# Optimization experiments

Measured on AMD Instinct MI355X. Metric: run time of the kernel, lower is better.

The kernel has to match this reference:

```python
import jax, jax.numpy as jnp
import numpy as np

N, D, H, E, K = 4096, 512, 2048, 8, 2  # tokens, input_size, hidden_size, num_experts, top_k


def setup_inputs() -> dict:
    key = jax.random.key(0)
    ks = jax.random.split(key, 4)
    x = jax.random.normal(ks[0], (N, D), dtype=jnp.float32)
    # torch init: weights ~ N(0, 0.001), biases zero
    Wg = jax.random.normal(ks[1], (D, E), dtype=jnp.float32) * 0.001
    bg = jnp.zeros((E,), jnp.float32)
    W1 = jax.random.normal(ks[2], (E, D, H), dtype=jnp.float32) * 0.001
    b1 = jnp.zeros((E, H), jnp.float32)
    W2 = jax.random.normal(ks[3], (E, H, D), dtype=jnp.float32) * 0.001
    b2 = jnp.zeros((E, D), jnp.float32)
    return {"x": x, "Wg": Wg, "bg": bg, "W1": W1, "b1": b1, "W2": W2, "b2": b2}


def reference(x, Wg, bg, W1, b1, W2, b2):
    # Gating: softmax over experts
    gates = jax.nn.softmax(x @ Wg + bg, axis=-1)            # [N, E]
    top_w, top_i = jax.lax.top_k(gates, K)                  # [N, K]
    top_w = top_w / jnp.sum(top_w, axis=-1, keepdims=True)  # renormalize

    # Expert MLP (fc1 -> fc2, no nonlinearity per source). Vectorized across all
    # experts, then gather the top-k selected outputs per token.
    h1 = jnp.einsum('nd,edh->neh', x, W1) + b1              # [N, E, H]
    all_out = jnp.einsum('neh,ehd->ned', h1, W2) + b2       # [N, E, D]
    sel = jnp.take_along_axis(all_out, top_i[:, :, None], axis=1)  # [N, K, D]

    combined = jnp.einsum('nkd,nk->nd', sel, top_w)         # [N, D]

    # usage counts: scatter-add of (detached) top-k weights per expert
    usage = jnp.zeros((E,), x.dtype).at[top_i.reshape(-1)].add(
        jax.lax.stop_gradient(top_w).reshape(-1))
    return combined, usage
```

## Files before the change

kernel.cpp:

```cpp
#include <hip/hip_runtime.h>
#include <hip/hip_bf16.h>


#define N_TOK 4096
#define DIM   512
#define HID   2048
#define NEXP  8
#define TOTSLOT (2 * N_TOK)
#define M1TILE 72
#define M2TILE 144
#define NGATE  256

typedef __attribute__((ext_vector_type(8))) short short8;
typedef __attribute__((ext_vector_type(4))) float f32x4;

static __device__ __forceinline__ unsigned short f2bf(float f) {
    __hip_bfloat16 b = __float2bfloat16(f);
    return *reinterpret_cast<unsigned short*>(&b);
}
static __device__ __forceinline__ float bf2f(unsigned short u) {
    return __uint_as_float((unsigned)u << 16);
}

static __device__ __forceinline__ void load16_to_lds(const void* g, void* l) {
    __builtin_amdgcn_global_load_lds(
        (const __attribute__((address_space(1))) unsigned int*)g,
        (__attribute__((address_space(3))) unsigned int*)l, 16, 0, 0);
}

__global__ __launch_bounds__(256) void prep_kernel(
    const float* __restrict__ W1, const float* __restrict__ W2,
    unsigned short* __restrict__ W1t, unsigned short* __restrict__ W2t,
    const float* __restrict__ x, const float* __restrict__ Wg,
    const float* __restrict__ bg,
    int* __restrict__ te, float* __restrict__ tw,
    int* __restrict__ pcnt, float* __restrict__ pus,
    unsigned short* __restrict__ Xb)
{
    int bid = blockIdx.x;
    int tid = threadIdx.x;

    if (bid < 4096) {
        __shared__ unsigned short tile[64][65];
        int z = bid >> 8, bx = bid & 255;
        const float* in; unsigned short* outp; int R, C, rt, ct, e;
        if (z < NEXP) { e = z;        in = W1; outp = W1t; R = DIM; C = HID; rt = bx >> 5; ct = bx & 31; }
        else          { e = z - NEXP; in = W2; outp = W2t; R = HID; C = DIM; rt = bx >> 3; ct = bx & 7;  }
        const float* src = in + (size_t)e * R * C;
        unsigned short* dst = outp + (size_t)e * R * C;
        int r0 = rt * 64, c0 = ct * 64;
        int rr = tid >> 2, cb = (tid & 3) * 16;
#pragma unroll
        for (int i = 0; i < 4; ++i) {
            float4 v = *(const float4*)&src[(size_t)(r0 + rr) * C + c0 + cb + i * 4];
            tile[rr][cb + i * 4 + 0] = f2bf(v.x);
            tile[rr][cb + i * 4 + 1] = f2bf(v.y);
            tile[rr][cb + i * 4 + 2] = f2bf(v.z);
            tile[rr][cb + i * 4 + 3] = f2bf(v.w);
        }
        __syncthreads();
#pragma unroll
        for (int i = 0; i < 4; ++i) {
            ushort4 u;
            u.x = tile[cb + i * 4 + 0][rr];
            u.y = tile[cb + i * 4 + 1][rr];
            u.z = tile[cb + i * 4 + 2][rr];
            u.w = tile[cb + i * 4 + 3][rr];
            *(ushort4*)&dst[(size_t)(c0 + rr) * R + r0 + cb + i * 4] = u;
        }
        return;
    }

    __shared__ int   lcnt[NEXP];
    __shared__ float lus[NEXP];
    int g = bid - 4096;
    if (tid < NEXP) { lcnt[tid] = 0; lus[tid] = 0.f; }
    __syncthreads();

    int wave = tid >> 6;
    int lane = tid & 63;

    for (int t = 0; t < 4; ++t) {
        int n = g * 16 + wave * 4 + t;

        float acc[NEXP];
#pragma unroll
        for (int e = 0; e < NEXP; ++e) acc[e] = 0.f;

#pragma unroll
        for (int it = 0; it < DIM / 64; ++it) {
            int d = it * 64 + lane;
            float xv = x[n * DIM + d];
            Xb[n * DIM + d] = f2bf(xv);
            float4 wa = *(const float4*)&Wg[d * NEXP];
            float4 wb = *(const float4*)&Wg[d * NEXP + 4];
            acc[0] += xv * wa.x; acc[1] += xv * wa.y;
            acc[2] += xv * wa.z; acc[3] += xv * wa.w;
            acc[4] += xv * wb.x; acc[5] += xv * wb.y;
            acc[6] += xv * wb.z; acc[7] += xv * wb.w;
        }
#pragma unroll
        for (int m = 32; m >= 1; m >>= 1) {
#pragma unroll
            for (int e = 0; e < NEXP; ++e)
                acc[e] += __shfl_xor(acc[e], m, 64);
        }
        if (lane == 0) {
            float l[NEXP];
#pragma unroll
            for (int e = 0; e < NEXP; ++e) l[e] = acc[e] + bg[e];
            int i0 = 0;
#pragma unroll
            for (int e = 1; e < NEXP; ++e) if (l[e] > l[i0]) i0 = e;
            int i1 = (i0 == 0) ? 1 : 0;
#pragma unroll
            for (int e = 0; e < NEXP; ++e)
                if (e != i0 && l[e] > l[i1]) i1 = e;
            float w0 = 1.f / (1.f + expf(l[i1] - l[i0]));
            float w1 = 1.f - w0;
            te[n * 2] = i0; te[n * 2 + 1] = i1;
            tw[n * 2] = w0; tw[n * 2 + 1] = w1;
            atomicAdd(&lcnt[i0], 1);
            atomicAdd(&lcnt[i1], 1);
            atomicAdd(&lus[i0], w0);
            atomicAdd(&lus[i1], w1);
        }
    }
    __syncthreads();
    if (tid < NEXP) {
        pcnt[g * NEXP + tid] = lcnt[tid];
        pus[g * NEXP + tid]  = lus[tid];
    }
}

__global__ __launch_bounds__(256) void scatter_kernel(
    int* __restrict__ te, const float* __restrict__ tw,
    const int* __restrict__ pcnt, const float* __restrict__ pus,
    int* __restrict__ btok, float* __restrict__ bwt,
    int* __restrict__ cnt, int* __restrict__ offs,
    int* __restrict__ tb128, int* __restrict__ tb64, int* __restrict__ ntile,
    float* __restrict__ usage)
{
    __shared__ int pc[NGATE * NEXP];
    __shared__ int cnt_s[NEXP], off_s[NEXP], base_s[NEXP], lrank[NEXP];
    int tid = threadIdx.x, b = blockIdx.x;

    {
        const int4* src = (const int4*)pcnt;
        int4* dst = (int4*)pc;
        dst[tid]       = src[tid];
        dst[tid + 256] = src[tid + 256];
    }
    if (tid < NEXP) lrank[tid] = 0;
    __syncthreads();

    if (tid < NEXP) {
        int e = tid, s = 0, pre = 0;
        for (int g = 0; g < NGATE; ++g) {
            int v = pc[g * NEXP + e];
            if (g < b * 16) pre += v;
            s += v;
        }
        cnt_s[e] = s; base_s[e] = pre;
    }
    __syncthreads();
    if (tid == 0) {
        int o = 0;
        for (int e = 0; e < NEXP; ++e) { off_s[e] = o; o += cnt_s[e]; }
    }
    __syncthreads();
    if (tid < NEXP) base_s[tid] += off_s[tid];

    if (b == 0) {
        if (tid < NEXP) {
            cnt[tid] = cnt_s[tid]; offs[tid] = off_s[tid];
            float s = 0.f;
            for (int g = 0; g < NGATE; ++g) s += pus[g * NEXP + tid];
            usage[tid] = s;
        }
        if (tid == 0) {
            int a = 0, bb = 0;
            for (int e = 0; e < NEXP; ++e) {
                tb128[e] = a; a += (cnt_s[e] + 127) >> 7;
                tb64[e]  = bb; bb += (cnt_s[e] + 63) >> 6;
            }
            tb128[NEXP] = a; tb64[NEXP] = bb;
            ntile[0] = a; ntile[1] = bb;
        }
    }
    __syncthreads();

    int n = b * 256 + tid;
    int e0 = te[n * 2], e1 = te[n * 2 + 1];
    int l0 = atomicAdd(&lrank[e0], 1);
    int l1 = atomicAdd(&lrank[e1], 1);
    int s0 = base_s[e0] + l0;
    int s1 = base_s[e1] + l1;
    btok[s0] = n; bwt[s0] = tw[n * 2];
    btok[s1] = n; bwt[s1] = tw[n * 2 + 1];
    te[n * 2] = s0; te[n * 2 + 1] = s1;
}


__global__ __launch_bounds__(256) void gemm1_kernel(
    const unsigned short* __restrict__ Xb, const unsigned short* __restrict__ W1t,
    const float* __restrict__ b1, const int* __restrict__ cnt,
    const int* __restrict__ offs, const int* __restrict__ btok,
    const int* __restrict__ tb128, const int* __restrict__ ntile,
    unsigned short* __restrict__ H1)
{
    __shared__ __align__(16) unsigned short Ws[2][128 * 64];
    __shared__ __align__(16) unsigned short Xs[2][128 * 64];
    __shared__ int tok_s[128];

    int bx = blockIdx.x;
    int ti = (bx & 7) * (M1TILE / 8) + (bx >> 3);
    if (ti >= ntile[0]) return;
    int e = 0;
#pragma unroll
    for (int k = 1; k < NEXP; ++k) if (ti >= tb128[k]) e = k;
    int tt = ti - tb128[e];
    int ht = blockIdx.y;
    int cn = cnt[e];
    int off_e = offs[e];
    int tid = threadIdx.x;

    if (tid < 128) {
        int lr = tt * 128 + tid;
        tok_s[tid] = (lr < cn) ? btok[off_e + lr] : 0;
    }
    __syncthreads();

    int wave = tid >> 6, lane = tid & 63;
    int mbase = (wave >> 1) * 64, nbase = (wave & 1) * 64;
    int quad = lane >> 4, lcol = lane & 15;
    f32x4 acc[4][4];
#pragma unroll
    for (int mi = 0; mi < 4; ++mi)
#pragma unroll
        for (int ni = 0; ni < 4; ++ni)
            acc[mi][ni] = (f32x4){0.f, 0.f, 0.f, 0.f};

    int Rb = tid >> 3, pc = tid & 7;
    const unsigned short* Wsrc = W1t + ((size_t)e * HID + ht * 128) * DIM;

    auto stage = [&](int buf, int k0) {
#pragma unroll
        for (int p = 0; p < 4; ++p) {
            int R = Rb + p * 32;
            int c = pc ^ (R & 7);
            load16_to_lds(&Wsrc[(size_t)R * DIM + k0 + c * 8], &Ws[buf][R * 64 + pc * 8]);
            load16_to_lds(&Xb[(size_t)tok_s[R] * DIM + k0 + c * 8], &Xs[buf][R * 64 + pc * 8]);
        }
    };

    stage(0, 0);

    const int NT = DIM / 64;
    for (int t = 0; t < NT; ++t) {
        int cur = t & 1;
        if (t + 1 < NT) {
            stage(cur ^ 1, (t + 1) * 64);
            asm volatile("s_waitcnt vmcnt(8)" ::: "memory");
        } else {
            asm volatile("s_waitcnt vmcnt(0)" ::: "memory");
        }
        __builtin_amdgcn_s_barrier();
        __builtin_amdgcn_sched_barrier(0);
#pragma unroll
        for (int h = 0; h < 2; ++h) {
            int cs = ((h * 4 + quad) ^ (lcol & 7)) * 8;
            short8 a[4], b[4];
#pragma unroll
            for (int i = 0; i < 4; ++i) {
                a[i] = *(const short8*)&Ws[cur][(mbase + i * 16 + lcol) * 64 + cs];
                b[i] = *(const short8*)&Xs[cur][(nbase + i * 16 + lcol) * 64 + cs];
            }
#pragma unroll
            for (int mi = 0; mi < 4; ++mi)
#pragma unroll
                for (int ni = 0; ni < 4; ++ni)
                    acc[mi][ni] = __builtin_amdgcn_mfma_f32_16x16x32_bf16(
                        a[mi], b[ni], acc[mi][ni], 0, 0, 0);
        }
        __builtin_amdgcn_sched_barrier(0);
        __builtin_amdgcn_s_barrier();
    }

    float4 bv[4];
#pragma unroll
    for (int mi = 0; mi < 4; ++mi)
        bv[mi] = *(const float4*)&b1[e * HID + ht * 128 + mbase + mi * 16 + quad * 4];
#pragma unroll
    for (int ni = 0; ni < 4; ++ni) {
        int tn = tt * 128 + nbase + ni * 16 + lcol;
        if (tn >= cn) continue;
        size_t srow = (size_t)(off_e + tn) * HID + ht * 128;
#pragma unroll
        for (int mi = 0; mi < 4; ++mi) {
            int hh = mbase + mi * 16 + quad * 4;
            ushort4 u;
            u.x = f2bf(acc[mi][ni][0] + bv[mi].x);
            u.y = f2bf(acc[mi][ni][1] + bv[mi].y);
            u.z = f2bf(acc[mi][ni][2] + bv[mi].z);
            u.w = f2bf(acc[mi][ni][3] + bv[mi].w);
            *(ushort4*)&H1[srow + hh] = u;
        }
    }
}

__global__ __launch_bounds__(256) void gemm2_kernel(
    const unsigned short* __restrict__ H1, const unsigned short* __restrict__ W2t,
    const float* __restrict__ b2, const int* __restrict__ cnt,
    const int* __restrict__ offs, const float* __restrict__ bwt,
    const int* __restrict__ tb64, const int* __restrict__ ntile,
    unsigned short* __restrict__ O)
{
    __shared__ __align__(16) unsigned short Ws[2][128 * 64];
    __shared__ __align__(16) unsigned short Hs[2][64 * 64];
    __shared__ float wt_s[64];

    int bx = blockIdx.x;
    int ti = (bx & 7) * (M2TILE / 8) + (bx >> 3);
    if (ti >= ntile[1]) return;
    int e = 0;
#pragma unroll
    for (int k = 1; k < NEXP; ++k) if (ti >= tb64[k]) e = k;
    int tt = ti - tb64[e];
    int dt = blockIdx.y;
    int cn = cnt[e];
    int off_e = offs[e];
    int sb = off_e + tt * 64;
    int tid = threadIdx.x;

    if (tid < 64) {
        int lr = tt * 64 + tid;
        wt_s[tid] = (lr < cn) ? bwt[off_e + lr] : 0.f;
    }

    int wave = tid >> 6, lane = tid & 63;
    int nbase = wave * 32;
    int quad = lane >> 4, lcol = lane & 15;
    f32x4 acc[4][2];
#pragma unroll
    for (int mi = 0; mi < 4; ++mi)
#pragma unroll
        for (int ni = 0; ni < 2; ++ni)
            acc[mi][ni] = (f32x4){0.f, 0.f, 0.f, 0.f};

    int Rb = tid >> 3, pc = tid & 7;
    const unsigned short* Wsrc = W2t + ((size_t)e * DIM + dt * 128) * HID;

    auto stage = [&](int buf, int k0) {
#pragma unroll
        for (int p = 0; p < 4; ++p) {
            int R = Rb + p * 32;
            int c = pc ^ (R & 7);
            load16_to_lds(&Wsrc[(size_t)R * HID + k0 + c * 8], &Ws[buf][R * 64 + pc * 8]);
        }
#pragma unroll
        for (int p = 0; p < 2; ++p) {
            int R = Rb + p * 32;
            int c = pc ^ (R & 7);
            int sr = sb + R; if (sr > TOTSLOT - 1) sr = TOTSLOT - 1;
            load16_to_lds(&H1[(size_t)sr * HID + k0 + c * 8], &Hs[buf][R * 64 + pc * 8]);
        }
    };

    stage(0, 0);

    const int NT = HID / 64;
    for (int t = 0; t < NT; ++t) {
        int cur = t & 1;
        if (t + 1 < NT) {
            stage(cur ^ 1, (t + 1) * 64);
            asm volatile("s_waitcnt vmcnt(6)" ::: "memory");
        } else {
            asm volatile("s_waitcnt vmcnt(0)" ::: "memory");
        }
        __builtin_amdgcn_s_barrier();
        __builtin_amdgcn_sched_barrier(0);
#pragma unroll
        for (int h = 0; h < 2; ++h) {
            int cs = ((h * 4 + quad) ^ (lcol & 7)) * 8;
            short8 a[4], b[2];
#pragma unroll
            for (int i = 0; i < 4; ++i)
                a[i] = *(const short8*)&Hs[cur][(i * 16 + lcol) * 64 + cs];
#pragma unroll
            for (int i = 0; i < 2; ++i)
                b[i] = *(const short8*)&Ws[cur][(nbase + i * 16 + lcol) * 64 + cs];
#pragma unroll
            for (int mi = 0; mi < 4; ++mi)
#pragma unroll
                for (int ni = 0; ni < 2; ++ni)
                    acc[mi][ni] = __builtin_amdgcn_mfma_f32_16x16x32_bf16(
                        a[mi], b[ni], acc[mi][ni], 0, 0, 0);
        }
        __builtin_amdgcn_sched_barrier(0);
        __builtin_amdgcn_s_barrier();
    }

    unsigned short* Oe = O + (size_t)sb * DIM + dt * 128;
#pragma unroll
    for (int ni = 0; ni < 2; ++ni) {
        int dl = nbase + ni * 16 + lcol;
        float bv = b2[e * DIM + dt * 128 + dl];
#pragma unroll
        for (int mi = 0; mi < 4; ++mi) {
            int rl = mi * 16 + quad * 4;
#pragma unroll
            for (int r = 0; r < 4; ++r) {
                int sl = rl + r;
                if (tt * 64 + sl < cn)
                    Oe[(size_t)sl * DIM + dl] = f2bf(wt_s[sl] * (acc[mi][ni][r] + bv));
            }
        }
    }
}

__global__ __launch_bounds__(256) void combine_kernel(
    const unsigned short* __restrict__ O, const int* __restrict__ sidx,
    float* __restrict__ out)
{
    int tid = threadIdx.x;
    int n = blockIdx.x * 2 + (tid >> 7);
    int dd = (tid & 127) * 4;
    int s0 = sidx[n * 2], s1 = sidx[n * 2 + 1];
    ushort4 a = *(const ushort4*)&O[(size_t)s0 * DIM + dd];
    ushort4 c = *(const ushort4*)&O[(size_t)s1 * DIM + dd];
    float4 o;
    o.x = bf2f(a.x) + bf2f(c.x);
    o.y = bf2f(a.y) + bf2f(c.y);
    o.z = bf2f(a.z) + bf2f(c.z);
    o.w = bf2f(a.w) + bf2f(c.w);
    *(float4*)&out[(size_t)n * DIM + dd] = o;
}

#define TN 16
#define HC 256
#define NCHUNK (HID / HC)

__global__ __launch_bounds__(256) void gating_fb_kernel(
    const float* __restrict__ x, const float* __restrict__ Wg,
    const float* __restrict__ bg,
    int* __restrict__ cnt, int* __restrict__ btok, float* __restrict__ bwt,
    float* __restrict__ usage)
{
    int wave = threadIdx.x >> 6;
    int lane = threadIdx.x & 63;
    int n = blockIdx.x * 4 + wave;
    float acc[NEXP];
#pragma unroll
    for (int e = 0; e < NEXP; ++e) acc[e] = 0.f;
    for (int d = lane; d < DIM; d += 64) {
        float xv = x[n * DIM + d];
        float4 wa = *(const float4*)&Wg[d * NEXP];
        float4 wb = *(const float4*)&Wg[d * NEXP + 4];
        acc[0] += xv * wa.x; acc[1] += xv * wa.y;
        acc[2] += xv * wa.z; acc[3] += xv * wa.w;
        acc[4] += xv * wb.x; acc[5] += xv * wb.y;
        acc[6] += xv * wb.z; acc[7] += xv * wb.w;
    }
#pragma unroll
    for (int m = 32; m >= 1; m >>= 1)
#pragma unroll
        for (int e = 0; e < NEXP; ++e)
            acc[e] += __shfl_xor(acc[e], m, 64);
    if (lane == 0) {
        float l[NEXP];
#pragma unroll
        for (int e = 0; e < NEXP; ++e) l[e] = acc[e] + bg[e];
        int i0 = 0;
#pragma unroll
        for (int e = 1; e < NEXP; ++e) if (l[e] > l[i0]) i0 = e;
        int i1 = (i0 == 0) ? 1 : 0;
#pragma unroll
        for (int e = 0; e < NEXP; ++e)
            if (e != i0 && l[e] > l[i1]) i1 = e;
        float w0 = 1.f / (1.f + expf(l[i1] - l[i0]));
        float w1 = 1.f - w0;
        int p0 = atomicAdd(&cnt[i0], 1);
        btok[i0 * N_TOK + p0] = n; bwt[i0 * N_TOK + p0] = w0;
        int p1 = atomicAdd(&cnt[i1], 1);
        btok[i1 * N_TOK + p1] = n; bwt[i1 * N_TOK + p1] = w1;
        atomicAdd(&usage[i0], w0);
        atomicAdd(&usage[i1], w1);
    }
}

__global__ __launch_bounds__(256) void expert_fb_kernel(
    const float* __restrict__ x, const float* __restrict__ W1,
    const float* __restrict__ b1, const float* __restrict__ W2,
    const float* __restrict__ b2, const int* __restrict__ cnt,
    const int* __restrict__ btok, const float* __restrict__ bwt,
    float* __restrict__ out)
{
    __shared__ float xs[TN][DIM];
    __shared__ float h1s[TN][HC];
    __shared__ int   tok_s[TN];
    __shared__ float wt_s[TN];
    int e = blockIdx.x >> 8;
    int tile = blockIdx.x & 255;
    int cn = cnt[e];
    int n0 = tile * TN;
    if (n0 >= cn) return;
    int nt = min(TN, cn - n0);
    int tid = threadIdx.x;
    if (tid < TN) {
        if (tid < nt) { tok_s[tid] = btok[e * N_TOK + n0 + tid]; wt_s[tid] = bwt[e * N_TOK + n0 + tid]; }
        else          { tok_s[tid] = 0; wt_s[tid] = 0.f; }
    }
    __syncthreads();
    for (int idx = tid; idx < TN * DIM; idx += 256) {
        int t = idx >> 9, d = idx & 511;
        xs[t][d] = (t < nt) ? x[tok_s[t] * DIM + d] : 0.f;
    }
    const float* W1e = W1 + (size_t)e * DIM * HID;
    const float* W2e = W2 + (size_t)e * HID * DIM;
    int tg = tid >> 6, lane = tid & 63;
    float oacc[4][8];
    {
        float4 ba = *(const float4*)&b2[e * DIM + lane * 8];
        float4 bb = *(const float4*)&b2[e * DIM + lane * 8 + 4];
#pragma unroll
        for (int ti = 0; ti < 4; ++ti) {
            oacc[ti][0] = ba.x; oacc[ti][1] = ba.y; oacc[ti][2] = ba.z; oacc[ti][3] = ba.w;
            oacc[ti][4] = bb.x; oacc[ti][5] = bb.y; oacc[ti][6] = bb.z; oacc[ti][7] = bb.w;
        }
    }
    __syncthreads();
    for (int ch = 0; ch < NCHUNK; ++ch) {
        int h0 = ch * HC;
        float f[4][4];
        {
            float4 b1v = *(const float4*)&b1[e * HID + h0 + lane * 4];
#pragma unroll
            for (int ti = 0; ti < 4; ++ti) {
                f[ti][0] = b1v.x; f[ti][1] = b1v.y; f[ti][2] = b1v.z; f[ti][3] = b1v.w;
            }
        }
        for (int d = 0; d < DIM; ++d) {
            float4 w1v = *(const float4*)&W1e[(size_t)d * HID + h0 + lane * 4];
#pragma unroll
            for (int ti = 0; ti < 4; ++ti) {
                float xv = xs[tg + 4 * ti][d];
                f[ti][0] += xv * w1v.x; f[ti][1] += xv * w1v.y;
                f[ti][2] += xv * w1v.z; f[ti][3] += xv * w1v.w;
            }
        }
        __syncthreads();
#pragma unroll
        for (int ti = 0; ti < 4; ++ti)
            *(float4*)&h1s[tg + 4 * ti][lane * 4] = make_float4(f[ti][0], f[ti][1], f[ti][2], f[ti][3]);
        __syncthreads();
        for (int j = 0; j < HC; ++j) {
            const float* w2row = &W2e[(size_t)(h0 + j) * DIM + lane * 8];
            float4 wa = *(const float4*)w2row;
            float4 wb = *(const float4*)(w2row + 4);
#pragma unroll
            for (int ti = 0; ti < 4; ++ti) {
                float hv = h1s[tg + 4 * ti][j];
                oacc[ti][0] += hv * wa.x; oacc[ti][1] += hv * wa.y;
                oacc[ti][2] += hv * wa.z; oacc[ti][3] += hv * wa.w;
                oacc[ti][4] += hv * wb.x; oacc[ti][5] += hv * wb.y;
                oacc[ti][6] += hv * wb.z; oacc[ti][7] += hv * wb.w;
            }
        }
    }
#pragma unroll
    for (int ti = 0; ti < 4; ++ti) {
        int t = tg + 4 * ti;
        if (t < nt) {
            float w = wt_s[t];
            float* o = &out[(size_t)tok_s[t] * DIM + lane * 8];
#pragma unroll
            for (int c = 0; c < 8; ++c)
                atomicAdd(&o[c], w * oacc[ti][c]);
        }
    }
}

extern "C" void kernel_launch(void* const* d_in, const int* in_sizes, int n_in,
                              void* d_out, int out_size, void* d_ws, size_t ws_size,
                              hipStream_t stream) {
    const float* x  = (const float*)d_in[0];
    const float* Wg = (const float*)d_in[1];
    const float* bg = (const float*)d_in[2];
    const float* W1 = (const float*)d_in[3];
    const float* b1 = (const float*)d_in[4];
    const float* W2 = (const float*)d_in[5];
    const float* b2 = (const float*)d_in[6];

    float* out   = (float*)d_out;
    float* usage = out + (size_t)N_TOK * DIM;

    char* ws = (char*)d_ws;
    int*   cnt   = (int*)(ws + 0);
    int*   offs  = (int*)(ws + 64);
    int*   tb128 = (int*)(ws + 128);
    int*   tb64  = (int*)(ws + 192);
    int*   ntile = (int*)(ws + 256);
    int*   pcnt  = (int*)(ws + 512);
    float* pus   = (float*)(ws + 8704);
    int*   te    = (int*)(ws + 16896);
    float* tw    = (float*)(ws + 49664);
    int*   btok  = (int*)(ws + 82432);
    float* bwt   = (float*)(ws + 115200);
    unsigned short* Xb  = (unsigned short*)(ws + 147968);
    unsigned short* W1t = (unsigned short*)(ws + 4342272);
    unsigned short* O   = W1t;
    unsigned short* W2t = (unsigned short*)(ws + 21119488);
    unsigned short* H1  = (unsigned short*)(ws + 37896704);
    const size_t WS_NEED = 71451136ULL;

    if (ws_size >= WS_NEED) {
        prep_kernel<<<4096 + NGATE, 256, 0, stream>>>(
            W1, W2, W1t, W2t, x, Wg, bg, te, tw, pcnt, pus, Xb);
        scatter_kernel<<<N_TOK / 256, 256, 0, stream>>>(
            te, tw, pcnt, pus, btok, bwt, cnt, offs, tb128, tb64, ntile, usage);
        gemm1_kernel<<<dim3(M1TILE, HID / 128), 256, 0, stream>>>(
            Xb, W1t, b1, cnt, offs, btok, tb128, ntile, H1);
        gemm2_kernel<<<dim3(M2TILE, DIM / 128), 256, 0, stream>>>(
            H1, W2t, b2, cnt, offs, bwt, tb64, ntile, O);
        combine_kernel<<<N_TOK / 2, 256, 0, stream>>>(O, te, out);
    } else {
        int*   fcnt  = (int*)d_ws;
        int*   fbtok = (int*)((char*)d_ws + 256);
        float* fbwt  = (float*)((char*)d_ws + 256 + (size_t)NEXP * N_TOK * sizeof(int));
        hipMemsetAsync(d_out, 0, (size_t)(N_TOK * DIM + NEXP) * sizeof(float), stream);
        hipMemsetAsync(d_ws, 0, 256, stream);
        gating_fb_kernel<<<N_TOK / 4, 256, 0, stream>>>(x, Wg, bg, fcnt, fbtok, fbwt, usage);
        expert_fb_kernel<<<NEXP * (N_TOK / TN), 256, 0, stream>>>(
            x, W1, b1, W2, b2, fcnt, fbtok, fbwt, out);
    }
}
```

Measured before the change: 209.8 us.

## Move W2 transpose into gemm1 launch and raise MFMA wave priority

The W2 fp32-to-bf16 transpose blocks move out of the prep kernel and become the first 2048 blocks of the gemm1 grid, so that conversion can overlap gemm1 compute instead of running before the scatter. The gemm1 grid is flattened to 1D to hold both block kinds. s_setprio(1) is also placed around the MFMA inner loops in both GEMMs so compute waves get issue priority over loader waves. The cost is an extra 64x65 LDS tile in gemm1, which may reduce occupancy, and transpose blocks that get scheduled ahead of GEMM tiles.

```diff
diff --git a/kernel.cpp b/kernel.cpp
--- a/kernel.cpp
+++ b/kernel.cpp
@@ -29,8 +29,7 @@
 }
 
 __global__ __launch_bounds__(256) void prep_kernel(
-    const float* __restrict__ W1, const float* __restrict__ W2,
-    unsigned short* __restrict__ W1t, unsigned short* __restrict__ W2t,
+    const float* __restrict__ W1, unsigned short* __restrict__ W1t,
     const float* __restrict__ x, const float* __restrict__ Wg,
     const float* __restrict__ bg,
     int* __restrict__ te, float* __restrict__ tw,
@@ -40,14 +39,13 @@
     int bid = blockIdx.x;
     int tid = threadIdx.x;
 
-    if (bid < 4096) {
+    if (bid < 2048) {
         __shared__ unsigned short tile[64][65];
-        int z = bid >> 8, bx = bid & 255;
-        const float* in; unsigned short* outp; int R, C, rt, ct, e;
-        if (z < NEXP) { e = z;        in = W1; outp = W1t; R = DIM; C = HID; rt = bx >> 5; ct = bx & 31; }
-        else          { e = z - NEXP; in = W2; outp = W2t; R = HID; C = DIM; rt = bx >> 3; ct = bx & 7;  }
-        const float* src = in + (size_t)e * R * C;
-        unsigned short* dst = outp + (size_t)e * R * C;
+        int e = bid >> 8, bx = bid & 255;
+        const int R = DIM, C = HID;
+        int rt = bx >> 5, ct = bx & 31;
+        const float* src = W1 + (size_t)e * R * C;
+        unsigned short* dst = W1t + (size_t)e * R * C;
         int r0 = rt * 64, c0 = ct * 64;
         int rr = tid >> 2, cb = (tid & 3) * 16;
 #pragma unroll
@@ -73,7 +71,7 @@
 
     __shared__ int   lcnt[NEXP];
     __shared__ float lus[NEXP];
-    int g = bid - 4096;
+    int g = bid - 2048;
     if (tid < NEXP) { lcnt[tid] = 0; lus[tid] = 0.f; }
     __syncthreads();
 
@@ -207,23 +205,57 @@
     const float* __restrict__ b1, const int* __restrict__ cnt,
     const int* __restrict__ offs, const int* __restrict__ btok,
     const int* __restrict__ tb128, const int* __restrict__ ntile,
-    unsigned short* __restrict__ H1)
+    unsigned short* __restrict__ H1,
+    const float* __restrict__ W2, unsigned short* __restrict__ W2t)
 {
     __shared__ __align__(16) unsigned short Ws[2][128 * 64];
     __shared__ __align__(16) unsigned short Xs[2][128 * 64];
     __shared__ int tok_s[128];
-
-    int bx = blockIdx.x;
-    int ti = (bx & 7) * (M1TILE / 8) + (bx >> 3);
+    __shared__ unsigned short tile[64][65];
+
+    int bid = blockIdx.x;
+    int tid = threadIdx.x;
+
+    if (bid < 2048) {
+        int e2 = bid >> 8, bx2 = bid & 255;
+        const int R = HID, C = DIM;
+        int rt = bx2 >> 3, ct = bx2 & 7;
+        const float* src = W2 + (size_t)e2 * R * C;
+        unsigned short* dst = W2t + (size_t)e2 * R * C;
+        int r0 = rt * 64, c0 = ct * 64;
+        int rr = tid >> 2, cb = (tid & 3) * 16;
+#pragma unroll
+        for (int i = 0; i < 4; ++i) {
+            float4 v = *(const float4*)&src[(size_t)(r0 + rr) * C + c0 + cb + i * 4];
+            tile[rr][cb + i * 4 + 0] = f2bf(v.x);
+            tile[rr][cb + i * 4 + 1] = f2bf(v.y);
+            tile[rr][cb + i * 4 + 2] = f2bf(v.z);
+            tile[rr][cb + i * 4 + 3] = f2bf(v.w);
+        }
+        __syncthreads();
+#pragma unroll
+        for (int i = 0; i < 4; ++i) {
+            ushort4 u;
+            u.x = tile[cb + i * 4 + 0][rr];
+            u.y = tile[cb + i * 4 + 1][rr];
+            u.z = tile[cb + i * 4 + 2][rr];
+            u.w = tile[cb + i * 4 + 3][rr];
+            *(ushort4*)&dst[(size_t)(c0 + rr) * R + r0 + cb + i * 4] = u;
+        }
+        return;
+    }
+
+    int id = bid - 2048;
+    int tix = id % M1TILE;
+    int ht = id / M1TILE;
+    int ti = (tix & 7) * (M1TILE / 8) + (tix >> 3);
     if (ti >= ntile[0]) return;
     int e = 0;
 #pragma unroll
     for (int k = 1; k < NEXP; ++k) if (ti >= tb128[k]) e = k;
     int tt = ti - tb128[e];
-    int ht = blockIdx.y;
     int cn = cnt[e];
     int off_e = offs[e];
-    int tid = threadIdx.x;
 
     if (tid < 128) {
         int lr = tt * 128 + tid;
@@ -267,6 +299,7 @@
         }
         __builtin_amdgcn_s_barrier();
         __builtin_amdgcn_sched_barrier(0);
+        __builtin_amdgcn_s_setprio(1);
 #pragma unroll
         for (int h = 0; h < 2; ++h) {
             int cs = ((h * 4 + quad) ^ (lcol & 7)) * 8;
@@ -283,6 +316,7 @@
                     acc[mi][ni] = __builtin_amdgcn_mfma_f32_16x16x32_bf16(
                         a[mi], b[ni], acc[mi][ni], 0, 0, 0);
         }
+        __builtin_amdgcn_s_setprio(0);
         __builtin_amdgcn_sched_barrier(0);
         __builtin_amdgcn_s_barrier();
     }
@@ -380,6 +414,7 @@
         }
         __builtin_amdgcn_s_barrier();
         __builtin_amdgcn_sched_barrier(0);
+        __builtin_amdgcn_s_setprio(1);
 #pragma unroll
         for (int h = 0; h < 2; ++h) {
             int cs = ((h * 4 + quad) ^ (lcol & 7)) * 8;
@@ -397,6 +432,7 @@
                     acc[mi][ni] = __builtin_amdgcn_mfma_f32_16x16x32_bf16(
                         a[mi], b[ni], acc[mi][ni], 0, 0, 0);
         }
+        __builtin_amdgcn_s_setprio(0);
         __builtin_amdgcn_sched_barrier(0);
         __builtin_amdgcn_s_barrier();
     }
@@ -615,12 +651,12 @@
     const size_t WS_NEED = 71451136ULL;
 
     if (ws_size >= WS_NEED) {
-        prep_kernel<<<4096 + NGATE, 256, 0, stream>>>(
-            W1, W2, W1t, W2t, x, Wg, bg, te, tw, pcnt, pus, Xb);
+        prep_kernel<<<2048 + NGATE, 256, 0, stream>>>(
+            W1, W1t, x, Wg, bg, te, tw, pcnt, pus, Xb);
         scatter_kernel<<<N_TOK / 256, 256, 0, stream>>>(
             te, tw, pcnt, pus, btok, bwt, cnt, offs, tb128, tb64, ntile, usage);
-        gemm1_kernel<<<dim3(M1TILE, HID / 128), 256, 0, stream>>>(
-            Xb, W1t, b1, cnt, offs, btok, tb128, ntile, H1);
+        gemm1_kernel<<<2048 + M1TILE * (HID / 128), 256, 0, stream>>>(
+            Xb, W1t, b1, cnt, offs, btok, tb128, ntile, H1, W2, W2t);
         gemm2_kernel<<<dim3(M2TILE, DIM / 128), 256, 0, stream>>>(
             H1, W2t, b2, cnt, offs, bwt, tb64, ntile, O);
         combine_kernel<<<N_TOK / 2, 256, 0, stream>>>(O, te, out);
```

Result: no change. 211.1 us (+0.6%).
